# Performance work log

Hardware: AMD Instinct MI355X
Metric: run time of the kernel (lower is better)

Reference implementation:

```python
import jax, jax.numpy as jnp
import numpy as np

N = 8192      # tokens
DIM = 1024    # model dim
E = 8         # num_experts
TOPK = 2      # min(2, num_experts)


def setup_inputs() -> dict:
    key = jax.random.key(0)
    ks = jax.random.split(key, 6)
    def w(k, shape, fan_in):
        return jax.random.normal(k, shape, jnp.float32) / np.float32(np.sqrt(fan_in))
    return {
        "x":   jax.random.normal(ks[0], (N, DIM), jnp.float32),
        # gate MLP: Linear(dim, 2*dim) -> SiLU -> Linear(2*dim, E)
        "Wg1": w(ks[1], (DIM, 2 * DIM), DIM),
        "bg1": jnp.zeros((2 * DIM,), jnp.float32),
        "Wg2": w(ks[2], (2 * DIM, E), 2 * DIM),
        "bg2": jnp.zeros((E,), jnp.float32),
        # experts: SHARED ff1 Linear(dim, 4*dim), per-expert ff2 Linear(4*dim, dim)
        "W1":  w(ks[3], (DIM, 4 * DIM), DIM),
        "b1":  jnp.zeros((4 * DIM,), jnp.float32),
        "W2":  w(ks[4], (E, 4 * DIM, DIM), 4 * DIM),
        "b2":  jnp.zeros((E, DIM), jnp.float32),
    }


def reference(x, Wg1, bg1, Wg2, bg2, W1, b1, W2, b2):
    # gate runs on detached input (x.detach())
    xg = jax.lax.stop_gradient(x)
    gates = jax.nn.silu(xg @ Wg1 + bg1) @ Wg2 + bg2          # [N, E]
    w, idx = jax.lax.top_k(gates, TOPK)                       # [N, K]
    w = jax.nn.softmax(w, axis=-1)                            # softmax over top-k weights
    # shared ff1 hidden, computed once for all experts
    h = jax.nn.silu(x @ W1 + b1)                              # [N, 4*DIM]
    # dense per-expert ff2 over the whole batch (matches original's full-batch expert compute)
    eo = jnp.einsum('nh,ehd->ned', h, W2) + b2                # [N, E, DIM]
    # dispatch/combine: gather selected experts per token, weight and sum
    sel = jnp.take_along_axis(eo, idx[:, :, None], axis=1)    # [N, K, DIM]
    return jnp.sum(w[:, :, None] * sel, axis=1)               # [N, DIM]
```

## Files before the change

kernel.cpp:

```cpp
#include <hip/hip_runtime.h>
#include <hip/hip_bf16.h>
#include <cstddef>

#define N_TOK 8192
#define DIM   1024
#define HG    2048
#define NE    8
#define HEXP  4096

#define BM 128
#define BN 128
#define BK 16

typedef __attribute__((ext_vector_type(8))) short bf16x8;
typedef __attribute__((ext_vector_type(4))) float f32x4;

__device__ __forceinline__ float silu_f(float z) {
    return z / (1.0f + expf(-z));
}

__device__ __forceinline__ unsigned short f2bf(float v) {
    unsigned u = __float_as_uint(v);
    unsigned r = (u + 0x7FFFu + ((u >> 16) & 1u)) >> 16;
    return (unsigned short)r;
}


__global__ __launch_bounds__(256) void conv_x(const float* __restrict__ src,
                                              unsigned short* __restrict__ dst)
{
    const size_t total = (size_t)N_TOK * DIM;
    size_t i = ((size_t)blockIdx.x * 256 + threadIdx.x) * 4;
    const size_t step = (size_t)gridDim.x * 256 * 4;
    for (; i + 3 < total; i += step) {
        float4 v = *(const float4*)(src + i);
        ushort4 o;
        o.x = f2bf(v.x); o.y = f2bf(v.y); o.z = f2bf(v.z); o.w = f2bf(v.w);
        *(ushort4*)(dst + i) = o;
    }
}

__global__ __launch_bounds__(256) void transpose_conv(const float* __restrict__ src,
                                                      unsigned short* __restrict__ dst,
                                                      int R, int C)
{
    __shared__ float tile[64][65];
    const size_t bofs = (size_t)blockIdx.z * R * C;
    const float* s = src + bofs;
    unsigned short* d = dst + bofs;
    const int r0 = blockIdx.y * 64, c0 = blockIdx.x * 64;
    const int t = threadIdx.x;
    #pragma unroll
    for (int i = 0; i < 16; i++) {
        int id = t + i * 256;
        int r = id >> 6, c = id & 63;
        tile[r][c] = s[(size_t)(r0 + r) * C + c0 + c];
    }
    __syncthreads();
    #pragma unroll
    for (int i = 0; i < 16; i++) {
        int id = t + i * 256;
        int c = id >> 6, r = id & 63;
        d[(size_t)(c0 + c) * R + r0 + r] = f2bf(tile[r][c]);
    }
}


__global__ __launch_bounds__(256) void gemm_bias_silu(
    const float* __restrict__ A, const float* __restrict__ B,
    const float* __restrict__ bias, float* __restrict__ C,
    int M, int Nc, int K)
{
    __shared__ float As[BK][BM];
    __shared__ float Bs[BK][BN];

    const int tid = threadIdx.x;
    const int tx = tid & 15;
    const int ty = tid >> 4;
    const int row0 = blockIdx.y * BM;
    const int col0 = blockIdx.x * BN;

    const int ar = tid >> 2;
    const int ac = (tid & 3) << 2;
    const int br = tid >> 5;
    const int bc = (tid & 31) << 2;

    const float* Ap = A + (size_t)(row0 + ar) * K + ac;
    const float* Bp = B + (size_t)br * Nc + col0 + bc;

    float acc[8][8];
    #pragma unroll
    for (int i = 0; i < 8; i++)
        #pragma unroll
        for (int j = 0; j < 8; j++) acc[i][j] = 0.0f;

    for (int k0 = 0; k0 < K; k0 += BK) {
        float4 a0 = *(const float4*)(Ap + k0);
        float4 a1 = *(const float4*)(Ap + k0 + (size_t)64 * K);
        float4 b0 = *(const float4*)(Bp + (size_t)k0 * Nc);
        float4 b1 = *(const float4*)(Bp + (size_t)(k0 + 8) * Nc);

        __syncthreads();
        As[ac + 0][ar] = a0.x; As[ac + 1][ar] = a0.y;
        As[ac + 2][ar] = a0.z; As[ac + 3][ar] = a0.w;
        As[ac + 0][ar + 64] = a1.x; As[ac + 1][ar + 64] = a1.y;
        As[ac + 2][ar + 64] = a1.z; As[ac + 3][ar + 64] = a1.w;
        *(float4*)&Bs[br][bc]     = b0;
        *(float4*)&Bs[br + 8][bc] = b1;
        __syncthreads();

        #pragma unroll
        for (int k = 0; k < BK; k++) {
            float a[8], b[8];
            *(float4*)&a[0] = *(const float4*)&As[k][ty * 8];
            *(float4*)&a[4] = *(const float4*)&As[k][ty * 8 + 4];
            *(float4*)&b[0] = *(const float4*)&Bs[k][tx * 8];
            *(float4*)&b[4] = *(const float4*)&Bs[k][tx * 8 + 4];
            #pragma unroll
            for (int i = 0; i < 8; i++)
                #pragma unroll
                for (int j = 0; j < 8; j++)
                    acc[i][j] = fmaf(a[i], b[j], acc[i][j]);
        }
    }

    #pragma unroll
    for (int i = 0; i < 8; i++) {
        const int row = row0 + ty * 8 + i;
        const int col = col0 + tx * 8;
        float4 o0, o1;
        o0.x = silu_f(acc[i][0] + bias[col + 0]);
        o0.y = silu_f(acc[i][1] + bias[col + 1]);
        o0.z = silu_f(acc[i][2] + bias[col + 2]);
        o0.w = silu_f(acc[i][3] + bias[col + 3]);
        o1.x = silu_f(acc[i][4] + bias[col + 4]);
        o1.y = silu_f(acc[i][5] + bias[col + 5]);
        o1.z = silu_f(acc[i][6] + bias[col + 6]);
        o1.w = silu_f(acc[i][7] + bias[col + 7]);
        *(float4*)&C[(size_t)row * Nc + col]     = o0;
        *(float4*)&C[(size_t)row * Nc + col + 4] = o1;
    }
}

__global__ __launch_bounds__(256) void gate2_topk(
    const float* __restrict__ g1, const float* __restrict__ Wg2,
    const float* __restrict__ bg2,
    unsigned* __restrict__ tok_list, float* __restrict__ w_list,
    unsigned* __restrict__ counts)
{
    const int wid  = threadIdx.x >> 6;
    const int lane = threadIdx.x & 63;
    const int t = blockIdx.x * 4 + wid;
    if (t >= N_TOK) return;

    float acc[NE];
    #pragma unroll
    for (int e = 0; e < NE; e++) acc[e] = 0.0f;

    const float* g = g1 + (size_t)t * HG;
    for (int k = lane; k < HG; k += 64) {
        const float gv = g[k];
        const float4 wa = *(const float4*)(Wg2 + (size_t)k * NE);
        const float4 wb = *(const float4*)(Wg2 + (size_t)k * NE + 4);
        acc[0] = fmaf(gv, wa.x, acc[0]);
        acc[1] = fmaf(gv, wa.y, acc[1]);
        acc[2] = fmaf(gv, wa.z, acc[2]);
        acc[3] = fmaf(gv, wa.w, acc[3]);
        acc[4] = fmaf(gv, wb.x, acc[4]);
        acc[5] = fmaf(gv, wb.y, acc[5]);
        acc[6] = fmaf(gv, wb.z, acc[6]);
        acc[7] = fmaf(gv, wb.w, acc[7]);
    }
    #pragma unroll
    for (int off = 32; off > 0; off >>= 1) {
        #pragma unroll
        for (int e = 0; e < NE; e++)
            acc[e] += __shfl_down(acc[e], off);
    }
    if (lane == 0) {
        float v0 = -3.4e38f, v1 = -3.4e38f;
        int i0 = 0, i1 = 0;
        #pragma unroll
        for (int e = 0; e < NE; e++) {
            const float v = acc[e] + bg2[e];
            if (v > v0) { v1 = v0; i1 = i0; v0 = v; i0 = e; }
            else if (v > v1) { v1 = v; i1 = e; }
        }
        const float e1 = expf(v1 - v0);
        const float inv = 1.0f / (1.0f + e1);
        const unsigned p0 = atomicAdd(&counts[i0], 1u);
        tok_list[i0 * N_TOK + p0] = (unsigned)t;
        w_list [i0 * N_TOK + p0] = inv;
        const unsigned p1 = atomicAdd(&counts[i1], 1u);
        tok_list[i1 * N_TOK + p1] = (unsigned)t;
        w_list [i1 * N_TOK + p1] = e1 * inv;
    }
}

__global__ void build_tiles(unsigned* __restrict__ meta,
                            unsigned* __restrict__ tile_e,
                            unsigned* __restrict__ tile_rs,
                            unsigned* __restrict__ tile_re)
{
    if (threadIdx.x == 0 && blockIdx.x == 0) {
        int nt = 0;
        for (int e = 0; e < NE; e++) {
            const unsigned c = meta[e];
            for (unsigned s = 0; s < c; s += 128) {
                tile_e[nt]  = (unsigned)e;
                tile_rs[nt] = (unsigned)(e * N_TOK) + s;
                unsigned re = s + 128; if (re > c) re = c;
                tile_re[nt] = (unsigned)(e * N_TOK) + re;
                nt++;
            }
        }
        meta[16] = (unsigned)nt;
    }
}


#define TBK 64

__global__ __launch_bounds__(256) void ff1_mfma(
    const unsigned short* __restrict__ Xb,
    const unsigned short* __restrict__ W1t,
    const float* __restrict__ b1,
    unsigned short* __restrict__ H)
{
    __shared__ __align__(16) unsigned short As[128][TBK];
    __shared__ __align__(16) unsigned short Bs[128][TBK];

    const int tid  = threadIdx.x;
    const int wave = tid >> 6;
    const int lane = tid & 63;
    const int wm = wave >> 1, wn = wave & 1;
    const int l15 = lane & 15;
    const int lk  = lane >> 4;
    const int row0 = blockIdx.y * 128;
    const int col0 = blockIdx.x * 128;

    f32x4 acc[4][4] = {};

    for (int k0 = 0; k0 < DIM; k0 += TBK) {
        __syncthreads();
        #pragma unroll
        for (int it = 0; it < 4; it++) {
            const int id = tid + it * 256;
            const int r = id >> 3, cb = id & 7;
            const int sb = (cb * 16) ^ ((r & 7) << 4);
            uint4 va = *(const uint4*)(Xb  + (size_t)(row0 + r) * DIM + k0 + cb * 8);
            uint4 vb = *(const uint4*)(W1t + (size_t)(col0 + r) * DIM + k0 + cb * 8);
            *(uint4*)((char*)&As[r][0] + sb) = va;
            *(uint4*)((char*)&Bs[r][0] + sb) = vb;
        }
        __syncthreads();

        #pragma unroll
        for (int ks = 0; ks < 2; ks++) {
            bf16x8 af[4], bfr[4];
            const int kb = (ks * 32 + lk * 8) * 2;
            #pragma unroll
            for (int mi = 0; mi < 4; mi++) {
                const int r = wm * 64 + mi * 16 + l15;
                af[mi] = *(const bf16x8*)((const char*)&As[r][0] + (kb ^ ((r & 7) << 4)));
            }
            #pragma unroll
            for (int ni = 0; ni < 4; ni++) {
                const int r = wn * 64 + ni * 16 + l15;
                bfr[ni] = *(const bf16x8*)((const char*)&Bs[r][0] + (kb ^ ((r & 7) << 4)));
            }
            #pragma unroll
            for (int mi = 0; mi < 4; mi++)
                #pragma unroll
                for (int ni = 0; ni < 4; ni++)
                    acc[mi][ni] = __builtin_amdgcn_mfma_f32_16x16x32_bf16(
                        af[mi], bfr[ni], acc[mi][ni], 0, 0, 0);
        }
    }

    #pragma unroll
    for (int ni = 0; ni < 4; ni++) {
        const int gc = col0 + wn * 64 + ni * 16 + l15;
        const float bv = b1[gc];
        #pragma unroll
        for (int mi = 0; mi < 4; mi++) {
            #pragma unroll
            for (int r = 0; r < 4; r++) {
                const int gr = row0 + wm * 64 + mi * 16 + lk * 4 + r;
                H[(size_t)gr * HEXP + gc] = f2bf(silu_f(acc[mi][ni][r] + bv));
            }
        }
    }
}

__global__ __launch_bounds__(256) void ff2_mfma(
    const unsigned short* __restrict__ Hb,
    const unsigned short* __restrict__ W2t,
    const float* __restrict__ b2,
    const unsigned* __restrict__ tok_list, const float* __restrict__ w_list,
    const unsigned* __restrict__ meta,
    const unsigned* __restrict__ tile_e, const unsigned* __restrict__ tile_rs,
    const unsigned* __restrict__ tile_re,
    float* __restrict__ out)
{
    const unsigned nt = meta[16];
    if (blockIdx.x >= nt) return;

    const int e  = (int)tile_e[blockIdx.x];
    const int rs = (int)tile_rs[blockIdx.x];
    const int re = (int)tile_re[blockIdx.x];
    const int col0 = blockIdx.y * 128;

    __shared__ __align__(16) unsigned short As[128][TBK];
    __shared__ __align__(16) unsigned short Bs[128][TBK];
    __shared__ unsigned tokr[128];

    const int tid  = threadIdx.x;
    const int wave = tid >> 6;
    const int lane = tid & 63;
    const int wm = wave >> 1, wn = wave & 1;
    const int l15 = lane & 15;
    const int lk  = lane >> 4;

    if (tid < 128)
        tokr[tid] = (rs + tid < re) ? tok_list[rs + tid] : tok_list[rs];

    const unsigned short* Bsrc = W2t + (size_t)e * DIM * HEXP;

    f32x4 acc[4][4] = {};

    for (int k0 = 0; k0 < HEXP; k0 += TBK) {
        __syncthreads();
        #pragma unroll
        for (int it = 0; it < 4; it++) {
            const int id = tid + it * 256;
            const int r = id >> 3, cb = id & 7;
            const int sb = (cb * 16) ^ ((r & 7) << 4);
            uint4 va = *(const uint4*)(Hb + (size_t)tokr[r] * HEXP + k0 + cb * 8);
            uint4 vb = *(const uint4*)(Bsrc + (size_t)(col0 + r) * HEXP + k0 + cb * 8);
            *(uint4*)((char*)&As[r][0] + sb) = va;
            *(uint4*)((char*)&Bs[r][0] + sb) = vb;
        }
        __syncthreads();

        #pragma unroll
        for (int ks = 0; ks < 2; ks++) {
            bf16x8 af[4], bfr[4];
            const int kb = (ks * 32 + lk * 8) * 2;
            #pragma unroll
            for (int mi = 0; mi < 4; mi++) {
                const int r = wm * 64 + mi * 16 + l15;
                af[mi] = *(const bf16x8*)((const char*)&As[r][0] + (kb ^ ((r & 7) << 4)));
            }
            #pragma unroll
            for (int ni = 0; ni < 4; ni++) {
                const int r = wn * 64 + ni * 16 + l15;
                bfr[ni] = *(const bf16x8*)((const char*)&Bs[r][0] + (kb ^ ((r & 7) << 4)));
            }
            #pragma unroll
            for (int mi = 0; mi < 4; mi++)
                #pragma unroll
                for (int ni = 0; ni < 4; ni++)
                    acc[mi][ni] = __builtin_amdgcn_mfma_f32_16x16x32_bf16(
                        af[mi], bfr[ni], acc[mi][ni], 0, 0, 0);
        }
    }

    #pragma unroll
    for (int ni = 0; ni < 4; ni++) {
        const int gc = col0 + wn * 64 + ni * 16 + l15;
        const float bv = b2[(size_t)e * DIM + gc];
        #pragma unroll
        for (int mi = 0; mi < 4; mi++) {
            #pragma unroll
            for (int r = 0; r < 4; r++) {
                const int lr = wm * 64 + mi * 16 + lk * 4 + r;
                if (rs + lr < re) {
                    const unsigned tok = tokr[lr];
                    const float w = w_list[rs + lr];
                    atomicAdd(out + (size_t)tok * DIM + gc, w * (acc[mi][ni][r] + bv));
                }
            }
        }
    }
}

extern "C" void kernel_launch(void* const* d_in, const int* in_sizes, int n_in,
                              void* d_out, int out_size, void* d_ws, size_t ws_size,
                              hipStream_t stream)
{
    const float* x   = (const float*)d_in[0];
    const float* Wg1 = (const float*)d_in[1];
    const float* bg1 = (const float*)d_in[2];
    const float* Wg2 = (const float*)d_in[3];
    const float* bg2 = (const float*)d_in[4];
    const float* W1  = (const float*)d_in[5];
    const float* b1  = (const float*)d_in[6];
    const float* W2  = (const float*)d_in[7];
    const float* b2  = (const float*)d_in[8];
    float* out = (float*)d_out;

    char* ws = (char*)d_ws;
    const size_t MB = 1024 * 1024;
    unsigned short* xb   = (unsigned short*)(ws);
    unsigned short* W1t  = (unsigned short*)(ws + 16 * MB);
    unsigned short* hbuf = (unsigned short*)(ws + 24 * MB);
    float*          g1   = (float*)        (ws + 88 * MB);
    unsigned short* W2t  = (unsigned short*)(ws + 88 * MB);
    unsigned* tok_list = (unsigned*)(ws + 152 * MB);
    float*    w_list   = (float*)   (ws + 152 * MB + 65536 * 4);
    unsigned* meta     = (unsigned*)(ws + 152 * MB + 65536 * 8);
    unsigned* tile_e   = meta + 1024;
    unsigned* tile_rs  = meta + 1280;
    unsigned* tile_re  = meta + 1536;

    (void)hipMemsetAsync(d_out, 0, (size_t)out_size * sizeof(float), stream);
    (void)hipMemsetAsync(meta, 0, 128, stream);

    const dim3 blk(256);
    conv_x<<<dim3(2048), blk, 0, stream>>>(x, xb);
    transpose_conv<<<dim3(HEXP / 64, DIM / 64, 1), blk, 0, stream>>>(W1, W1t, DIM, HEXP);
    gemm_bias_silu<<<dim3(HG / BN, N_TOK / BM), blk, 0, stream>>>(
        x, Wg1, bg1, g1, N_TOK, HG, DIM);
    gate2_topk<<<dim3(N_TOK / 4), blk, 0, stream>>>(
        g1, Wg2, bg2, tok_list, w_list, meta);
    build_tiles<<<dim3(1), dim3(64), 0, stream>>>(meta, tile_e, tile_rs, tile_re);
    ff1_mfma<<<dim3(HEXP / 128, N_TOK / 128), blk, 0, stream>>>(xb, W1t, b1, hbuf);
    transpose_conv<<<dim3(DIM / 64, HEXP / 64, NE), blk, 0, stream>>>(W2, W2t, HEXP, DIM);
    ff2_mfma<<<dim3(N_TOK * 2 / 128 + NE, DIM / 128), blk, 0, stream>>>(
        hbuf, W2t, b2, tok_list, w_list, meta, tile_e, tile_rs, tile_re, out);
}
```

Measured before the change: 1.326 ms.

## Run gate GEMM in bf16 MFMA and recompute ambiguous tokens in fp32

The fp32 SIMT gate GEMM (x @ Wg1) is replaced by the bf16 MFMA kernel shared with ff1, which writes the gate hidden activations as bf16. Tokens whose second and third gate scores lie within a fixed margin are flagged and their gate path is recomputed in fp32, so top-2 selection stays exact. This removes the dominant fp32 FLOP cost of the gate, but adds a Wg1 transpose/conversion, two extra launches, and recompute cost that grows with the number of flagged tokens.

```diff
diff --git a/kernel.cpp b/kernel.cpp
--- a/kernel.cpp
+++ b/kernel.cpp
@@ -11,6 +11,7 @@
 #define BM 128
 #define BN 128
 #define BK 16
+#define THETA 0.05f
 
 typedef __attribute__((ext_vector_type(8))) short bf16x8;
 typedef __attribute__((ext_vector_type(4))) float f32x4;
@@ -23,6 +24,10 @@
     unsigned u = __float_as_uint(v);
     unsigned r = (u + 0x7FFFu + ((u >> 16) & 1u)) >> 16;
     return (unsigned short)r;
+}
+
+__device__ __forceinline__ float bf2f(unsigned short v) {
+    return __uint_as_float((unsigned)v << 16);
 }
 
 
@@ -66,27 +71,180 @@
 }
 
 
-__global__ __launch_bounds__(256) void gemm_bias_silu(
-    const float* __restrict__ A, const float* __restrict__ B,
-    const float* __restrict__ bias, float* __restrict__ C,
-    int M, int Nc, int K)
-{
+#define TBK 64
+
+__global__ __launch_bounds__(256) void gemm_bf16_silu(
+    const unsigned short* __restrict__ A,
+    const unsigned short* __restrict__ Bt,
+    const float* __restrict__ bias,
+    unsigned short* __restrict__ C,
+    int Nc)
+{
+    __shared__ __align__(16) unsigned short As[128][TBK];
+    __shared__ __align__(16) unsigned short Bs[128][TBK];
+
+    const int tid  = threadIdx.x;
+    const int wave = tid >> 6;
+    const int lane = tid & 63;
+    const int wm = wave >> 1, wn = wave & 1;
+    const int l15 = lane & 15;
+    const int lk  = lane >> 4;
+    const int row0 = blockIdx.y * 128;
+    const int col0 = blockIdx.x * 128;
+
+    f32x4 acc[4][4] = {};
+
+    for (int k0 = 0; k0 < DIM; k0 += TBK) {
+        __syncthreads();
+        #pragma unroll
+        for (int it = 0; it < 4; it++) {
+            const int id = tid + it * 256;
+            const int r = id >> 3, cb = id & 7;
+            const int sb = (cb * 16) ^ ((r & 7) << 4);
+            uint4 va = *(const uint4*)(A  + (size_t)(row0 + r) * DIM + k0 + cb * 8);
+            uint4 vb = *(const uint4*)(Bt + (size_t)(col0 + r) * DIM + k0 + cb * 8);
+            *(uint4*)((char*)&As[r][0] + sb) = va;
+            *(uint4*)((char*)&Bs[r][0] + sb) = vb;
+        }
+        __syncthreads();
+
+        #pragma unroll
+        for (int ks = 0; ks < 2; ks++) {
+            bf16x8 af[4], bfr[4];
+            const int kb = (ks * 32 + lk * 8) * 2;
+            #pragma unroll
+            for (int mi = 0; mi < 4; mi++) {
+                const int r = wm * 64 + mi * 16 + l15;
+                af[mi] = *(const bf16x8*)((const char*)&As[r][0] + (kb ^ ((r & 7) << 4)));
+            }
+            #pragma unroll
+            for (int ni = 0; ni < 4; ni++) {
+                const int r = wn * 64 + ni * 16 + l15;
+                bfr[ni] = *(const bf16x8*)((const char*)&Bs[r][0] + (kb ^ ((r & 7) << 4)));
+            }
+            #pragma unroll
+            for (int mi = 0; mi < 4; mi++)
+                #pragma unroll
+                for (int ni = 0; ni < 4; ni++)
+                    acc[mi][ni] = __builtin_amdgcn_mfma_f32_16x16x32_bf16(
+                        af[mi], bfr[ni], acc[mi][ni], 0, 0, 0);
+        }
+    }
+
+    #pragma unroll
+    for (int ni = 0; ni < 4; ni++) {
+        const int gc = col0 + wn * 64 + ni * 16 + l15;
+        const float bv = bias[gc];
+        #pragma unroll
+        for (int mi = 0; mi < 4; mi++) {
+            #pragma unroll
+            for (int r = 0; r < 4; r++) {
+                const int gr = row0 + wm * 64 + mi * 16 + lk * 4 + r;
+                C[(size_t)gr * Nc + gc] = f2bf(silu_f(acc[mi][ni][r] + bv));
+            }
+        }
+    }
+}
+
+
+__global__ __launch_bounds__(256) void gate2_topk_flag(
+    const unsigned short* __restrict__ g1b, const float* __restrict__ Wg2,
+    const float* __restrict__ bg2,
+    unsigned* __restrict__ tok_list, float* __restrict__ w_list,
+    unsigned* __restrict__ meta, unsigned* __restrict__ flaglist)
+{
+    const int wid  = threadIdx.x >> 6;
+    const int lane = threadIdx.x & 63;
+    const int t = blockIdx.x * 4 + wid;
+    if (t >= N_TOK) return;
+
+    float acc[NE];
+    #pragma unroll
+    for (int e = 0; e < NE; e++) acc[e] = 0.0f;
+
+    const unsigned short* g = g1b + (size_t)t * HG;
+    for (int kb = lane * 8; kb < HG; kb += 512) {
+        ushort4 ga = *(const ushort4*)(g + kb);
+        ushort4 gb = *(const ushort4*)(g + kb + 4);
+        float gv[8];
+        gv[0] = bf2f(ga.x); gv[1] = bf2f(ga.y); gv[2] = bf2f(ga.z); gv[3] = bf2f(ga.w);
+        gv[4] = bf2f(gb.x); gv[5] = bf2f(gb.y); gv[6] = bf2f(gb.z); gv[7] = bf2f(gb.w);
+        #pragma unroll
+        for (int j = 0; j < 8; j++) {
+            const float4 wa = *(const float4*)(Wg2 + (size_t)(kb + j) * NE);
+            const float4 wb = *(const float4*)(Wg2 + (size_t)(kb + j) * NE + 4);
+            acc[0] = fmaf(gv[j], wa.x, acc[0]);
+            acc[1] = fmaf(gv[j], wa.y, acc[1]);
+            acc[2] = fmaf(gv[j], wa.z, acc[2]);
+            acc[3] = fmaf(gv[j], wa.w, acc[3]);
+            acc[4] = fmaf(gv[j], wb.x, acc[4]);
+            acc[5] = fmaf(gv[j], wb.y, acc[5]);
+            acc[6] = fmaf(gv[j], wb.z, acc[6]);
+            acc[7] = fmaf(gv[j], wb.w, acc[7]);
+        }
+    }
+    #pragma unroll
+    for (int off = 32; off > 0; off >>= 1) {
+        #pragma unroll
+        for (int e = 0; e < NE; e++)
+            acc[e] += __shfl_down(acc[e], off);
+    }
+    if (lane == 0) {
+        float v0 = -3.4e38f, v1 = -3.4e38f, v2 = -3.4e38f;
+        int i0 = 0, i1 = 0;
+        #pragma unroll
+        for (int e = 0; e < NE; e++) {
+            const float v = acc[e] + bg2[e];
+            if (v > v0)      { v2 = v1; v1 = v0; i1 = i0; v0 = v; i0 = e; }
+            else if (v > v1) { v2 = v1; v1 = v; i1 = e; }
+            else if (v > v2) { v2 = v; }
+        }
+        if (v1 - v2 < THETA) {
+            const unsigned p = atomicAdd(&meta[17], 1u);
+            flaglist[p] = (unsigned)t;
+        } else {
+            const float e1 = expf(v1 - v0);
+            const float inv = 1.0f / (1.0f + e1);
+            const unsigned p0 = atomicAdd(&meta[i0], 1u);
+            tok_list[i0 * N_TOK + p0] = (unsigned)t;
+            w_list [i0 * N_TOK + p0] = inv;
+            const unsigned p1 = atomicAdd(&meta[i1], 1u);
+            tok_list[i1 * N_TOK + p1] = (unsigned)t;
+            w_list [i1 * N_TOK + p1] = e1 * inv;
+        }
+    }
+}
+
+__global__ __launch_bounds__(256) void regate_gemm(
+    const float* __restrict__ x, const float* __restrict__ Wg1,
+    const float* __restrict__ bg1,
+    const unsigned* __restrict__ flaglist, const unsigned* __restrict__ meta,
+    float* __restrict__ g1f)
+{
+    const int nflag = (int)meta[17];
+    const int rs = blockIdx.y * BM;
+    if (rs >= nflag) return;
+    const int re = (rs + BM < nflag) ? rs + BM : nflag;
+    const int col0 = blockIdx.x * BN;
+
     __shared__ float As[BK][BM];
     __shared__ float Bs[BK][BN];
 
     const int tid = threadIdx.x;
     const int tx = tid & 15;
     const int ty = tid >> 4;
-    const int row0 = blockIdx.y * BM;
-    const int col0 = blockIdx.x * BN;
-
     const int ar = tid >> 2;
     const int ac = (tid & 3) << 2;
     const int br = tid >> 5;
     const int bc = (tid & 31) << 2;
 
-    const float* Ap = A + (size_t)(row0 + ar) * K + ac;
-    const float* Bp = B + (size_t)br * Nc + col0 + bc;
+    const int r0 = rs + ar;
+    const int r1 = rs + ar + 64;
+    const unsigned t0 = flaglist[(r0 < re) ? r0 : rs];
+    const unsigned t1 = flaglist[(r1 < re) ? r1 : rs];
+    const float* A0 = x + (size_t)t0 * DIM + ac;
+    const float* A1 = x + (size_t)t1 * DIM + ac;
+    const float* Bp = Wg1 + (size_t)br * HG + col0 + bc;
 
     float acc[8][8];
     #pragma unroll
@@ -94,11 +252,11 @@
         #pragma unroll
         for (int j = 0; j < 8; j++) acc[i][j] = 0.0f;
 
-    for (int k0 = 0; k0 < K; k0 += BK) {
-        float4 a0 = *(const float4*)(Ap + k0);
-        float4 a1 = *(const float4*)(Ap + k0 + (size_t)64 * K);
-        float4 b0 = *(const float4*)(Bp + (size_t)k0 * Nc);
-        float4 b1 = *(const float4*)(Bp + (size_t)(k0 + 8) * Nc);
+    for (int k0 = 0; k0 < DIM; k0 += BK) {
+        const float4 a0 = *(const float4*)(A0 + k0);
+        const float4 a1 = *(const float4*)(A1 + k0);
+        const float4 b0 = *(const float4*)(Bp + (size_t)k0 * HG);
+        const float4 b1 = *(const float4*)(Bp + (size_t)(k0 + 8) * HG);
 
         __syncthreads();
         As[ac + 0][ar] = a0.x; As[ac + 1][ar] = a0.y;
@@ -126,38 +284,35 @@
 
     #pragma unroll
     for (int i = 0; i < 8; i++) {
-        const int row = row0 + ty * 8 + i;
-        const int col = col0 + tx * 8;
-        float4 o0, o1;
-        o0.x = silu_f(acc[i][0] + bias[col + 0]);
-        o0.y = silu_f(acc[i][1] + bias[col + 1]);
-        o0.z = silu_f(acc[i][2] + bias[col + 2]);
-        o0.w = silu_f(acc[i][3] + bias[col + 3]);
-        o1.x = silu_f(acc[i][4] + bias[col + 4]);
-        o1.y = silu_f(acc[i][5] + bias[col + 5]);
-        o1.z = silu_f(acc[i][6] + bias[col + 6]);
-        o1.w = silu_f(acc[i][7] + bias[col + 7]);
-        *(float4*)&C[(size_t)row * Nc + col]     = o0;
-        *(float4*)&C[(size_t)row * Nc + col + 4] = o1;
-    }
-}
-
-__global__ __launch_bounds__(256) void gate2_topk(
-    const float* __restrict__ g1, const float* __restrict__ Wg2,
+        const int row = rs + ty * 8 + i;
+        if (row < re) {
+            const int col = col0 + tx * 8;
+            #pragma unroll
+            for (int j = 0; j < 8; j++)
+                g1f[(size_t)row * HG + col + j] = silu_f(acc[i][j] + bg1[col + j]);
+        }
+    }
+}
+
+__global__ __launch_bounds__(256) void regate_top2(
+    const float* __restrict__ g1f, const float* __restrict__ Wg2,
     const float* __restrict__ bg2,
+    const unsigned* __restrict__ flaglist,
     unsigned* __restrict__ tok_list, float* __restrict__ w_list,
-    unsigned* __restrict__ counts)
+    unsigned* __restrict__ meta)
 {
     const int wid  = threadIdx.x >> 6;
     const int lane = threadIdx.x & 63;
-    const int t = blockIdx.x * 4 + wid;
-    if (t >= N_TOK) return;
+    const int f = blockIdx.x * 4 + wid;
+    const int nflag = (int)meta[17];
+    if (f >= nflag) return;
+    const unsigned t = flaglist[f];
 
     float acc[NE];
     #pragma unroll
     for (int e = 0; e < NE; e++) acc[e] = 0.0f;
 
-    const float* g = g1 + (size_t)t * HG;
+    const float* g = g1f + (size_t)f * HG;
     for (int k = lane; k < HG; k += 64) {
         const float gv = g[k];
         const float4 wa = *(const float4*)(Wg2 + (size_t)k * NE);
@@ -188,10 +343,10 @@
         }
         const float e1 = expf(v1 - v0);
         const float inv = 1.0f / (1.0f + e1);
-        const unsigned p0 = atomicAdd(&counts[i0], 1u);
+        const unsigned p0 = atomicAdd(&meta[i0], 1u);
         tok_list[i0 * N_TOK + p0] = (unsigned)t;
         w_list [i0 * N_TOK + p0] = inv;
-        const unsigned p1 = atomicAdd(&counts[i1], 1u);
+        const unsigned p1 = atomicAdd(&meta[i1], 1u);
         tok_list[i1 * N_TOK + p1] = (unsigned)t;
         w_list [i1 * N_TOK + p1] = e1 * inv;
     }
@@ -218,81 +373,6 @@
     }
 }
 
-
-#define TBK 64
-
-__global__ __launch_bounds__(256) void ff1_mfma(
-    const unsigned short* __restrict__ Xb,
-    const unsigned short* __restrict__ W1t,
-    const float* __restrict__ b1,
-    unsigned short* __restrict__ H)
-{
-    __shared__ __align__(16) unsigned short As[128][TBK];
-    __shared__ __align__(16) unsigned short Bs[128][TBK];
-
-    const int tid  = threadIdx.x;
-    const int wave = tid >> 6;
-    const int lane = tid & 63;
-    const int wm = wave >> 1, wn = wave & 1;
-    const int l15 = lane & 15;
-    const int lk  = lane >> 4;
-    const int row0 = blockIdx.y * 128;
-    const int col0 = blockIdx.x * 128;
-
-    f32x4 acc[4][4] = {};
-
-    for (int k0 = 0; k0 < DIM; k0 += TBK) {
-        __syncthreads();
-        #pragma unroll
-        for (int it = 0; it < 4; it++) {
-            const int id = tid + it * 256;
-            const int r = id >> 3, cb = id & 7;
-            const int sb = (cb * 16) ^ ((r & 7) << 4);
-            uint4 va = *(const uint4*)(Xb  + (size_t)(row0 + r) * DIM + k0 + cb * 8);
-            uint4 vb = *(const uint4*)(W1t + (size_t)(col0 + r) * DIM + k0 + cb * 8);
-            *(uint4*)((char*)&As[r][0] + sb) = va;
-            *(uint4*)((char*)&Bs[r][0] + sb) = vb;
-        }
-        __syncthreads();
-
-        #pragma unroll
-        for (int ks = 0; ks < 2; ks++) {
-            bf16x8 af[4], bfr[4];
-            const int kb = (ks * 32 + lk * 8) * 2;
-            #pragma unroll
-            for (int mi = 0; mi < 4; mi++) {
-                const int r = wm * 64 + mi * 16 + l15;
-                af[mi] = *(const bf16x8*)((const char*)&As[r][0] + (kb ^ ((r & 7) << 4)));
-            }
-            #pragma unroll
-            for (int ni = 0; ni < 4; ni++) {
-                const int r = wn * 64 + ni * 16 + l15;
-                bfr[ni] = *(const bf16x8*)((const char*)&Bs[r][0] + (kb ^ ((r & 7) << 4)));
-            }
-            #pragma unroll
-            for (int mi = 0; mi < 4; mi++)
-                #pragma unroll
-                for (int ni = 0; ni < 4; ni++)
-                    acc[mi][ni] = __builtin_amdgcn_mfma_f32_16x16x32_bf16(
-                        af[mi], bfr[ni], acc[mi][ni], 0, 0, 0);
-        }
-    }
-
-    #pragma unroll
-    for (int ni = 0; ni < 4; ni++) {
-        const int gc = col0 + wn * 64 + ni * 16 + l15;
-        const float bv = b1[gc];
-        #pragma unroll
-        for (int mi = 0; mi < 4; mi++) {
-            #pragma unroll
-            for (int r = 0; r < 4; r++) {
-                const int gr = row0 + wm * 64 + mi * 16 + lk * 4 + r;
-                H[(size_t)gr * HEXP + gc] = f2bf(silu_f(acc[mi][ni][r] + bv));
-            }
-        }
-    }
-}
-
 __global__ __launch_bounds__(256) void ff2_mfma(
     const unsigned short* __restrict__ Hb,
     const unsigned short* __restrict__ W2t,
@@ -404,28 +484,35 @@
     const size_t MB = 1024 * 1024;
     unsigned short* xb   = (unsigned short*)(ws);
     unsigned short* W1t  = (unsigned short*)(ws + 16 * MB);
-    unsigned short* hbuf = (unsigned short*)(ws + 24 * MB);
-    float*          g1   = (float*)        (ws + 88 * MB);
-    unsigned short* W2t  = (unsigned short*)(ws + 88 * MB);
-    unsigned* tok_list = (unsigned*)(ws + 152 * MB);
-    float*    w_list   = (float*)   (ws + 152 * MB + 65536 * 4);
-    unsigned* meta     = (unsigned*)(ws + 152 * MB + 65536 * 8);
+    unsigned short* Wg1t = (unsigned short*)(ws + 24 * MB);
+    unsigned short* g1b  = (unsigned short*)(ws + 28 * MB);
+    float*          g1f  = (float*)        (ws + 28 * MB);
+    unsigned short* hbuf = (unsigned short*)(ws + 28 * MB);
+    unsigned short* W2t  = (unsigned short*)(ws + 92 * MB);
+    unsigned* tok_list = (unsigned*)(ws + 156 * MB);
+    float*    w_list   = (float*)   (ws + 156 * MB + 65536 * 4);
+    unsigned* meta     = (unsigned*)(ws + 156 * MB + 65536 * 8);
     unsigned* tile_e   = meta + 1024;
     unsigned* tile_rs  = meta + 1280;
     unsigned* tile_re  = meta + 1536;
+    unsigned* flaglist = meta + 2048;
 
     (void)hipMemsetAsync(d_out, 0, (size_t)out_size * sizeof(float), stream);
     (void)hipMemsetAsync(meta, 0, 128, stream);
 
     const dim3 blk(256);
     conv_x<<<dim3(2048), blk, 0, stream>>>(x, xb);
+    transpose_conv<<<dim3(HG / 64, DIM / 64, 1), blk, 0, stream>>>(Wg1, Wg1t, DIM, HG);
+    gemm_bf16_silu<<<dim3(HG / 128, N_TOK / 128), blk, 0, stream>>>(xb, Wg1t, bg1, g1b, HG);
+    gate2_topk_flag<<<dim3(N_TOK / 4), blk, 0, stream>>>(
+        g1b, Wg2, bg2, tok_list, w_list, meta, flaglist);
+    regate_gemm<<<dim3(HG / BN, N_TOK / BM), blk, 0, stream>>>(
+        x, Wg1, bg1, flaglist, meta, g1f);
+    regate_top2<<<dim3(N_TOK / 4), blk, 0, stream>>>(
+        g1f, Wg2, bg2, flaglist, tok_list, w_list, meta);
+    build_tiles<<<dim3(1), dim3(64), 0, stream>>>(meta, tile_e, tile_rs, tile_re);
     transpose_conv<<<dim3(HEXP / 64, DIM / 64, 1), blk, 0, stream>>>(W1, W1t, DIM, HEXP);
-    gemm_bias_silu<<<dim3(HG / BN, N_TOK / BM), blk, 0, stream>>>(
-        x, Wg1, bg1, g1, N_TOK, HG, DIM);
-    gate2_topk<<<dim3(N_TOK / 4), blk, 0, stream>>>(
-        g1, Wg2, bg2, tok_list, w_list, meta);
-    build_tiles<<<dim3(1), dim3(64), 0, stream>>>(meta, tile_e, tile_rs, tile_re);
-    ff1_mfma<<<dim3(HEXP / 128, N_TOK / 128), blk, 0, stream>>>(xb, W1t, b1, hbuf);
+    gemm_bf16_silu<<<dim3(HEXP / 128, N_TOK / 128), blk, 0, stream>>>(xb, W1t, b1, hbuf, HEXP);
     transpose_conv<<<dim3(DIM / 64, HEXP / 64, NE), blk, 0, stream>>>(W2, W2t, HEXP, DIM);
     ff2_mfma<<<dim3(N_TOK * 2 / 128 + NE, DIM / 128), blk, 0, stream>>>(
         hbuf, W2t, b2, tok_list, w_list, meta, tile_e, tile_rs, tile_re, out);
```

Result: faster. 1.129 ms (-14.9%).
